# Optimization experiments

Measured on AMD Instinct MI355X. Metric: run time of the kernel, lower is better.

The kernel has to match this reference:

```python
import jax, jax.numpy as jnp
import numpy as np

B, IN_SIZE, OUT_SIZE, N_QUBITS, DEPTH = 4096, 512, 256, 12, 3
C64 = jnp.complex64
BN_EPS = 1e-5


def setup_inputs() -> dict:
    key = jax.random.key(0)
    ks = jax.random.split(key, 6)
    x = jax.random.normal(ks[0], (B, IN_SIZE), jnp.float32)
    enc_w = jax.random.normal(ks[1], (N_QUBITS, IN_SIZE), jnp.float32) / np.sqrt(IN_SIZE)
    enc_b = jnp.zeros((N_QUBITS,), jnp.float32)
    rot_params = jax.random.normal(ks[2], (DEPTH, N_QUBITS, 3), jnp.float32) * 0.1
    ent_params = jax.random.normal(ks[3], (DEPTH, N_QUBITS - 1), jnp.float32) * 0.1
    dec_w = jax.random.normal(ks[4], (OUT_SIZE, N_QUBITS), jnp.float32) / np.sqrt(N_QUBITS)
    dec_b = jnp.zeros((OUT_SIZE,), jnp.float32)
    return {
        'x': x, 'enc_w': enc_w, 'enc_b': enc_b,
        'rot_params': rot_params, 'ent_params': ent_params,
        'dec_w': dec_w, 'dec_b': dec_b,
        'bn1_gamma': jnp.ones((N_QUBITS,), jnp.float32),
        'bn1_beta': jnp.zeros((N_QUBITS,), jnp.float32),
        'bn2_gamma': jnp.ones((OUT_SIZE,), jnp.float32),
        'bn2_beta': jnp.zeros((OUT_SIZE,), jnp.float32),
    }


def _m2(a, b, c, d):
    return jnp.stack([jnp.stack([a, b]), jnp.stack([c, d])]).astype(C64)


def _rx(t):
    c = jnp.cos(t / 2).astype(C64)
    s = jnp.sin(t / 2).astype(C64)
    return _m2(c, -1j * s, -1j * s, c)


def _ry(t):
    c = jnp.cos(t / 2)
    s = jnp.sin(t / 2)
    return _m2(c, -s, s, c)


def _rz(p):
    z = jnp.zeros((), C64)
    return _m2(jnp.exp(-1j * p / 2), z, z, jnp.exp(1j * p / 2))


def _apply_1q(state, U, q):
    # state: [B, 2^n]; apply 2x2 U on qubit q (qubit 0 = most significant axis)
    b = state.shape[0]
    s = state.reshape(b, 2 ** q, 2, -1)
    s = jnp.einsum('ij,bkjl->bkil', U, s)
    return s.reshape(b, -1)


def _apply_cry(state, theta, q):
    # controlled-Ry: control qubit q, target qubit q+1 (adjacent)
    b = state.shape[0]
    R = _ry(theta)
    st = state.reshape(b, 2 ** q, 2, 2, -1)
    s0 = st[:, :, 0]
    s1 = jnp.einsum('ij,bkjl->bkil', R, st[:, :, 1])
    return jnp.stack([s0, s1], axis=2).reshape(b, -1)


def _batchnorm(x, g, b):
    # BatchNorm1d in training mode: biased batch stats
    m = x.mean(0)
    v = x.var(0)
    return g * (x - m) / jnp.sqrt(v + BN_EPS) + b


def _quantum_forward(encoded, rot_params, ent_params):
    # Batched statevector simulation of the per-sample circuit.
    b, n = encoded.shape
    depth = rot_params.shape[0]
    # amplitude encoding: normalize, theta = 2*arcsin(clip(|a|,0,1)), P(pi) if a<0
    norm = jnp.linalg.norm(encoded, axis=1, keepdims=True)
    a = jnp.where(norm > 0, encoded / jnp.maximum(norm, 1e-30), encoded)
    amp = jnp.clip(jnp.abs(a), 0.0, 1.0)              # sin(theta/2)
    cos_h = jnp.sqrt(jnp.maximum(1.0 - amp * amp, 0.0))  # cos(theta/2)
    sgn = jnp.where(a < 0, -1.0, 1.0)                  # P(pi) flips sign of |1> amp
    qvec = jnp.stack([cos_h, sgn * amp], axis=-1).astype(C64)  # [B, n, 2]
    # product state via successive outer products (loop over fixed n qubits)
    state = jnp.ones((b, 1), C64)
    for q in range(n):
        state = (state[:, :, None] * qvec[:, q, None, :]).reshape(b, -1)
    # parameterized circuit
    for l in range(depth):
        for q in range(n):
            U = _rz(rot_params[l, q, 2]) @ _ry(rot_params[l, q, 1]) @ _rx(rot_params[l, q, 0])
            state = _apply_1q(state, U, q)
        for q in range(n - 1):
            state = _apply_cry(state, ent_params[l, q], q)
    # per-qubit P(|1>) measurement probabilities
    idx = jnp.arange(2 ** n)
    bits = ((idx[:, None] >> (n - 1 - jnp.arange(n))) & 1).astype(jnp.float32)  # [2^n, n]
    probs = (jnp.abs(state) ** 2).astype(jnp.float32) @ bits  # [B, n]
    return probs


def reference(x, enc_w, enc_b, rot_params, ent_params, dec_w, dec_b,
              bn1_gamma, bn1_beta, bn2_gamma, bn2_beta):
    encoded = x @ enc_w.T + enc_b
    encoded = jnp.tanh(_batchnorm(encoded, bn1_gamma, bn1_beta))
    probs = _quantum_forward(encoded, rot_params, ent_params)
    out = probs @ dec_w.T + dec_b
    return _batchnorm(out, bn2_gamma, bn2_beta)
```

## Files before the change

### kernel.cpp

```cpp
#include <hip/hip_runtime.h>

#define BATCH   4096
#define IN_SZ   512
#define NQ      12
#define OUT_SZ  256
#define DEPTH   3
#define NST     4096
#define BN_EPS  1e-5f

#define OFF_ENC    0
#define OFF_BN1M   49152
#define OFF_BN1R   49168
#define OFF_GU     49184
#define OFF_GC     49472
#define OFF_GF     49568
#define OFF_PROBS  49792
#define OFF_PMEAN  98944
#define OFF_COV    98960
#define OFF_GG     99104

typedef float v2f __attribute__((ext_vector_type(2)));
typedef float v4f __attribute__((ext_vector_type(4)));
#define SW2(a) __builtin_shufflevector(a, a, 1, 0)

__global__ void k_encode(const float* __restrict__ x, const float* __restrict__ w,
                         const float* __restrict__ bvec,
                         const float* __restrict__ rot, const float* __restrict__ ent,
                         float* __restrict__ enc, float* __restrict__ gU, float* __restrict__ gC,
                         float* __restrict__ gF, float* __restrict__ gG) {
    if (blockIdx.x == 1024) {
        int t = threadIdx.x;
        if (t < DEPTH * NQ) {
            float ax = rot[t * 3 + 0] * 0.5f;
            float ay = rot[t * 3 + 1] * 0.5f;
            float az = rot[t * 3 + 2] * 0.5f;
            float cx = cosf(ax), sx = sinf(ax);
            float cy = cosf(ay), sy = sinf(ay);
            float cz = cosf(az), sz = sinf(az);
            float m00r =  cy * cx, m00i =  sy * sx;
            float m01r = -sy * cx, m01i = -cy * sx;
            float m10r =  sy * cx, m10i = -cy * sx;
            float m11r =  cy * cx, m11i = -sy * sx;
            float* o = gU + t * 8;
            o[0] = cz * m00r + sz * m00i;  o[1] = cz * m00i - sz * m00r;
            o[2] = cz * m01r + sz * m01i;  o[3] = cz * m01i - sz * m01r;
            o[4] = cz * m10r - sz * m10i;  o[5] = cz * m10i + sz * m10r;
            o[6] = cz * m11r - sz * m11i;  o[7] = cz * m11i + sz * m11r;
        }
        if (t >= 64 && t - 64 < DEPTH * (NQ - 1)) {
            int i = t - 64;
            float th = ent[i] * 0.5f;
            gC[i * 2 + 0] = cosf(th);
            gC[i * 2 + 1] = sinf(th);
        }
        if (t >= 128 && t - 128 < DEPTH * 9) {
            int i = t - 128;
            int l = i / 9, k = i % 9;
            int c = k + k / 3;
            int tq = c + 1;
            const float* rr = rot + (l * NQ + tq) * 3;
            float ax = rr[0] * 0.5f, ay = rr[1] * 0.5f, az = rr[2] * 0.5f;
            float cx = cosf(ax), sx = sinf(ax);
            float cy = cosf(ay), sy = sinf(ay);
            float cz = cosf(az), sz = sinf(az);
            float m00r =  cy * cx, m00i =  sy * sx;
            float m01r = -sy * cx, m01i = -cy * sx;
            float m10r =  sy * cx, m10i = -cy * sx;
            float m11r =  cy * cx, m11i = -sy * sx;
            float u0 = cz * m00r + sz * m00i, u1 = cz * m00i - sz * m00r;
            float u2 = cz * m01r + sz * m01i, u3 = cz * m01i - sz * m01r;
            float u4 = cz * m10r - sz * m10i, u5 = cz * m10i + sz * m10r;
            float u6 = cz * m11r - sz * m11i, u7 = cz * m11i + sz * m11r;
            float th = ent[l * (NQ - 1) + c] * 0.5f;
            float c_ = cosf(th), s_ = sinf(th);
            float* o = gF + i * 8;
            o[0] = c_ * u0 - s_ * u4;  o[1] = c_ * u1 - s_ * u5;
            o[2] = c_ * u2 - s_ * u6;  o[3] = c_ * u3 - s_ * u7;
            o[4] = s_ * u0 + c_ * u4;  o[5] = s_ * u1 + c_ * u5;
            o[6] = s_ * u2 + c_ * u6;  o[7] = s_ * u3 + c_ * u7;
        }
        if (t >= 160 && t - 160 < DEPTH * 2) {
            int i = t - 160;
            int l = i >> 1;
            int c = (i & 1) ? 7 : 3;
            int tq = c + 1;
            const float* rr = rot + (l * NQ + tq) * 3;
            float ax = rr[0] * 0.5f, ay = rr[1] * 0.5f, az = rr[2] * 0.5f;
            float cx = cosf(ax), sx = sinf(ax);
            float cy = cosf(ay), sy = sinf(ay);
            float cz = cosf(az), sz = sinf(az);
            float m00r =  cy * cx, m00i =  sy * sx;
            float m01r = -sy * cx, m01i = -cy * sx;
            float m10r =  sy * cx, m10i = -cy * sx;
            float m11r =  cy * cx, m11i = -sy * sx;
            float u0 = cz * m00r + sz * m00i, u1 = cz * m00i - sz * m00r;
            float u2 = cz * m01r + sz * m01i, u3 = cz * m01i - sz * m01r;
            float u4 = cz * m10r - sz * m10i, u5 = cz * m10i + sz * m10r;
            float u6 = cz * m11r - sz * m11i, u7 = cz * m11i + sz * m11r;
            float th = ent[l * (NQ - 1) + c] * 0.5f;
            float c_ = cosf(th), s_ = sinf(th);
            float* o = gG + (l * 2 + (i & 1)) * 8;
            o[0] = c_ * u0 - s_ * u4;  o[1] = c_ * u1 - s_ * u5;
            o[2] = c_ * u2 - s_ * u6;  o[3] = c_ * u3 - s_ * u7;
            o[4] = s_ * u0 + c_ * u4;  o[5] = s_ * u1 + c_ * u5;
            o[6] = s_ * u2 + c_ * u6;  o[7] = s_ * u3 + c_ * u7;
        }
        return;
    }
    int t = threadIdx.x;
    int wv = t >> 6, lane = t & 63;
    int row = blockIdx.x * 4 + wv;
    const float4* xr = (const float4*)(x + row * IN_SZ) + lane * 2;
    float4 xa = xr[0], xb = xr[1];
    float acc[NQ];
    #pragma unroll
    for (int q = 0; q < NQ; q++) {
        const float4* wr = (const float4*)(w + q * IN_SZ) + lane * 2;
        float4 wa = wr[0], wb = wr[1];
        float d = xa.x*wa.x + xa.y*wa.y + xa.z*wa.z + xa.w*wa.w
                + xb.x*wb.x + xb.y*wb.y + xb.z*wb.z + xb.w*wb.w;
        #pragma unroll
        for (int o = 32; o > 0; o >>= 1) d += __shfl_down(d, o, 64);
        acc[q] = d;
    }
    if (lane == 0) {
        float* er = enc + row * NQ;
        #pragma unroll
        for (int q = 0; q < NQ; q++) er[q] = acc[q] + bvec[q];
    }
}

__device__ float blockAllSum(float v, float* scr) {
    #pragma unroll
    for (int o = 32; o > 0; o >>= 1) v += __shfl_down(v, o, 64);
    int lane = threadIdx.x & 63, w = threadIdx.x >> 6;
    __syncthreads();
    if (lane == 0) scr[w] = v;
    __syncthreads();
    return scr[0] + scr[1] + scr[2] + scr[3];
}

__global__ void k_bnstats(const float* __restrict__ xm, float* __restrict__ mo,
                          float* __restrict__ ro) {
    __shared__ float scr[32];
    int j = blockIdx.x, t = threadIdx.x;
    float s = 0.f, s2 = 0.f;
    for (int b = t; b < BATCH; b += 1024) {
        float v = xm[b * NQ + j];
        s += v; s2 += v * v;
    }
    #pragma unroll
    for (int o = 32; o > 0; o >>= 1) { s += __shfl_down(s, o, 64); s2 += __shfl_down(s2, o, 64); }
    int lane = t & 63, w = t >> 6;
    if (lane == 0) { scr[w] = s; scr[16 + w] = s2; }
    __syncthreads();
    if (t == 0) {
        float S = 0.f, S2 = 0.f;
        #pragma unroll
        for (int i = 0; i < 16; i++) { S += scr[i]; S2 += scr[16 + i]; }
        float mean = S / (float)BATCH;
        float var  = S2 / (float)BATCH - mean * mean;
        mo[j] = mean;
        ro[j] = 1.f / sqrtf(var + BN_EPS);
    }
}

#define SLA2(j) ((T << 4) | ((((j) ^ ((T >> 1) & 7))) << 1))
#define SLB(m)  (((T & 0xF0) << 4) | ((m) << 4) | ((T & 15) ^ ((m) & 14)))
#define SLC(m)  (((m) << 8) | (T ^ ((((T >> 5) & 7)) << 1)))

#define LDA(j, Ra, Rb) { v4f t_ = *(const v4f*)(xch + SLA2(j));                 \
    Ra = __builtin_shufflevector(t_, t_, 0, 1);                                 \
    Rb = __builtin_shufflevector(t_, t_, 2, 3); }
#define STA(j, Ra, Rb) { v4f t_ = __builtin_shufflevector(Ra, Rb, 0, 1, 2, 3);  \
    *(v4f*)(xch + SLA2(j)) = t_; }

#define LOADA do { LDA(0,s0,s1) LDA(1,s2,s3) LDA(2,s4,s5) LDA(3,s6,s7)          \
    LDA(4,s8,s9) LDA(5,s10,s11) LDA(6,s12,s13) LDA(7,s14,s15) } while (0)
#define STORA do { STA(0,s0,s1) STA(1,s2,s3) STA(2,s4,s5) STA(3,s6,s7)          \
    STA(4,s8,s9) STA(5,s10,s11) STA(6,s12,s13) STA(7,s14,s15) } while (0)

#define LOADW(SL) do {                                                          \
    s0=xch[SL(0)];  s1=xch[SL(1)];  s2=xch[SL(2)];  s3=xch[SL(3)];              \
    s4=xch[SL(4)];  s5=xch[SL(5)];  s6=xch[SL(6)];  s7=xch[SL(7)];              \
    s8=xch[SL(8)];  s9=xch[SL(9)];  s10=xch[SL(10)]; s11=xch[SL(11)];           \
    s12=xch[SL(12)]; s13=xch[SL(13)]; s14=xch[SL(14)]; s15=xch[SL(15)]; } while (0)
#define STORW(SL) do {                                                          \
    xch[SL(0)]=s0;  xch[SL(1)]=s1;  xch[SL(2)]=s2;  xch[SL(3)]=s3;              \
    xch[SL(4)]=s4;  xch[SL(5)]=s5;  xch[SL(6)]=s6;  xch[SL(7)]=s7;              \
    xch[SL(8)]=s8;  xch[SL(9)]=s9;  xch[SL(10)]=s10; xch[SL(11)]=s11;           \
    xch[SL(12)]=s12; xch[SL(13)]=s13; xch[SL(14)]=s14; xch[SL(15)]=s15; } while (0)

#define U_LOADP(uptr) const float* u_ = (uptr);                                  \
    v2f c00r = {u_[0], u_[0]}, c00i = {-u_[1], u_[1]};                           \
    v2f c01r = {u_[2], u_[2]}, c01i = {-u_[3], u_[3]};                           \
    v2f c10r = {u_[4], u_[4]}, c10i = {-u_[5], u_[5]};                           \
    v2f c11r = {u_[6], u_[6]}, c11i = {-u_[7], u_[7]};

#define U_LOADF(uptr) const float* f_ = (uptr);                                  \
    v2f d00r = {f_[0], f_[0]}, d00i = {-f_[1], f_[1]};                           \
    v2f d01r = {f_[2], f_[2]}, d01i = {-f_[3], f_[3]};                           \
    v2f d10r = {f_[4], f_[4]}, d10i = {-f_[5], f_[5]};                           \
    v2f d11r = {f_[6], f_[6]}, d11i = {-f_[7], f_[7]};

#define U_LOADSEL(uptr, gptr, cond) const float* u_ = (uptr);                    \
    const float* g_ = (gptr); int k_ = (cond);                                   \
    float e0_ = k_ ? g_[0] : u_[0], e1_ = k_ ? g_[1] : u_[1];                    \
    float e2_ = k_ ? g_[2] : u_[2], e3_ = k_ ? g_[3] : u_[3];                    \
    float e4_ = k_ ? g_[4] : u_[4], e5_ = k_ ? g_[5] : u_[5];                    \
    float e6_ = k_ ? g_[6] : u_[6], e7_ = k_ ? g_[7] : u_[7];                    \
    v2f c00r = {e0_, e0_}, c00i = {-e1_, e1_};                                   \
    v2f c01r = {e2_, e2_}, c01i = {-e3_, e3_};                                   \
    v2f c10r = {e4_, e4_}, c10i = {-e5_, e5_};                                   \
    v2f c11r = {e6_, e6_}, c11i = {-e7_, e7_};

#define U_PAIRP(A, B) { v2f a0 = A, a1 = B, a0s = SW2(a0), a1s = SW2(a1);        \
    A = a0*c00r + a0s*c00i + a1*c01r + a1s*c01i;                                 \
    B = a0*c10r + a0s*c10i + a1*c11r + a1s*c11i; }

#define U_PAIRF(A, B) { v2f a0 = A, a1 = B, a0s = SW2(a0), a1s = SW2(a1);        \
    A = a0*d00r + a0s*d00i + a1*d01r + a1s*d01i;                                 \
    B = a0*d10r + a0s*d10i + a1*d11r + a1s*d11i; }

#define APPLY_U_K3(uptr) do { U_LOADP(uptr)                                      \
    U_PAIRP(s0,s8) U_PAIRP(s1,s9) U_PAIRP(s2,s10) U_PAIRP(s3,s11)                \
    U_PAIRP(s4,s12) U_PAIRP(s5,s13) U_PAIRP(s6,s14) U_PAIRP(s7,s15) } while (0)

#define APPLY_USEL_K3(uptr, gptr, cond) do { U_LOADSEL(uptr, gptr, cond)         \
    U_PAIRP(s0,s8) U_PAIRP(s1,s9) U_PAIRP(s2,s10) U_PAIRP(s3,s11)                \
    U_PAIRP(s4,s12) U_PAIRP(s5,s13) U_PAIRP(s6,s14) U_PAIRP(s7,s15) } while (0)

#define APPLY_UF_K2(uP, uF) do { U_LOADP(uP) U_LOADF(uF)                         \
    U_PAIRP(s0,s4) U_PAIRP(s1,s5) U_PAIRP(s2,s6) U_PAIRP(s3,s7)                  \
    U_PAIRF(s8,s12) U_PAIRF(s9,s13) U_PAIRF(s10,s14) U_PAIRF(s11,s15) } while (0)
#define APPLY_UF_K1(uP, uF) do { U_LOADP(uP) U_LOADF(uF)                         \
    U_PAIRP(s0,s2) U_PAIRP(s1,s3) U_PAIRF(s4,s6) U_PAIRF(s5,s7)                  \
    U_PAIRP(s8,s10) U_PAIRP(s9,s11) U_PAIRF(s12,s14) U_PAIRF(s13,s15) } while (0)
#define APPLY_UF_K0(uP, uF) do { U_LOADP(uP) U_LOADF(uF)                         \
    U_PAIRP(s0,s1) U_PAIRF(s2,s3) U_PAIRP(s4,s5) U_PAIRF(s6,s7)                  \
    U_PAIRP(s8,s9) U_PAIRF(s10,s11) U_PAIRP(s12,s13) U_PAIRF(s14,s15) } while (0)

#define PRJ(S) ((S).x*(S).x + (S).y*(S).y)
#define WREDUCE(v) { v += __shfl_down(v,32,64); v += __shfl_down(v,16,64);       \
    v += __shfl_down(v,8,64); v += __shfl_down(v,4,64);                          \
    v += __shfl_down(v,2,64); v += __shfl_down(v,1,64); }

__launch_bounds__(256)
__global__ void k_quantum(const float* __restrict__ enc,
                          const float* __restrict__ bn1m, const float* __restrict__ bn1r,
                          const float* __restrict__ g1, const float* __restrict__ b1,
                          const float* __restrict__ gU, const float* __restrict__ gC,
                          const float* __restrict__ gF, const float* __restrict__ gG,
                          float* __restrict__ probs) {
    __shared__ __align__(16) v2f xch[NST];

    int T = threadIdx.x, b = blockIdx.x;

    float* qv = (float*)xch;
    if (T < 16) {
        float h = 0.f;
        if (T < NQ) {
            h = tanhf(g1[T] * (enc[b * NQ + T] - bn1m[T]) * bn1r[T] + b1[T]);
        }
        float n2 = h * h;
        n2 += __shfl_xor(n2, 1, 16);
        n2 += __shfl_xor(n2, 2, 16);
        n2 += __shfl_xor(n2, 4, 16);
        n2 += __shfl_xor(n2, 8, 16);
        float norm = sqrtf(n2);
        bool  nz   = norm > 0.f;
        float rinv = 1.f / fmaxf(norm, 1e-30f);
        float a_   = nz ? h * rinv : h;
        float amp_ = fminf(fabsf(a_), 1.f);
        float qc   = sqrtf(fmaxf(1.f - amp_ * amp_, 0.f));
        float qs   = (a_ < 0.f) ? -amp_ : amp_;
        if (T < NQ) { qv[T * 2] = qc; qv[T * 2 + 1] = qs; }
    }
    __syncthreads();
    float qc0 = qv[0],  qs0 = qv[1],  qc1 = qv[2],  qs1 = qv[3];
    float qc2 = qv[4],  qs2 = qv[5],  qc3 = qv[6],  qs3 = qv[7];
    float qc4 = qv[8],  qs4 = qv[9],  qc5 = qv[10], qs5 = qv[11];
    float qc6 = qv[12], qs6 = qv[13], qc7 = qv[14], qs7 = qv[15];
    float qc8 = qv[16], qs8 = qv[17], qc9 = qv[18], qs9 = qv[19];
    float qc10 = qv[20], qs10 = qv[21], qc11 = qv[22], qs11 = qv[23];
    __syncthreads();

    v2f s0, s1, s2, s3, s4, s5, s6, s7, s8, s9, s10, s11, s12, s13, s14, s15;

    {
        float f = ((T>>7)&1 ? qs4 : qc4) * ((T>>6)&1 ? qs5 : qc5)
                * ((T>>5)&1 ? qs6 : qc6) * ((T>>4)&1 ? qs7 : qc7)
                * ((T>>3)&1 ? qs8 : qc8) * ((T>>2)&1 ? qs9 : qc9)
                * ((T>>1)&1 ? qs10 : qc10) * ((T>>0)&1 ? qs11 : qc11);
        float p0c = f * qc0,  p0s = f * qs0;
        float p00 = p0c*qc1, p01 = p0c*qs1, p10 = p0s*qc1, p11 = p0s*qs1;
        float q000 = p00*qc2, q001 = p00*qs2, q010 = p01*qc2, q011 = p01*qs2;
        float q100 = p10*qc2, q101 = p10*qs2, q110 = p11*qc2, q111 = p11*qs2;
        s0  = (v2f){q000*qc3, 0.f};  s1  = (v2f){q000*qs3, 0.f};
        s2  = (v2f){q001*qc3, 0.f};  s3  = (v2f){q001*qs3, 0.f};
        s4  = (v2f){q010*qc3, 0.f};  s5  = (v2f){q010*qs3, 0.f};
        s6  = (v2f){q011*qc3, 0.f};  s7  = (v2f){q011*qs3, 0.f};
        s8  = (v2f){q100*qc3, 0.f};  s9  = (v2f){q100*qs3, 0.f};
        s10 = (v2f){q101*qc3, 0.f};  s11 = (v2f){q101*qs3, 0.f};
        s12 = (v2f){q110*qc3, 0.f};  s13 = (v2f){q110*qs3, 0.f};
        s14 = (v2f){q111*qc3, 0.f};  s15 = (v2f){q111*qs3, 0.f};
        APPLY_U_K3(gU + 0 * 8);
        APPLY_UF_K2(gU + 1 * 8, gF + 0 * 8);
        APPLY_UF_K1(gU + 2 * 8, gF + 1 * 8);
        APPLY_UF_K0(gU + 3 * 8, gF + 2 * 8);
        STORW(SLC);
    }
    __syncthreads();

    #pragma unroll 1
    for (int l = 0; l < DEPTH; l++) {
        const float* UL = gU + l * 96;
        const float* FL = gF + l * 72;
        const float* GL = gG + l * 16;
        LOADW(SLB);
        APPLY_USEL_K3(UL + 4 * 8, GL + 0, T & 16);
        APPLY_UF_K2(UL + 5 * 8, FL + 3 * 8);
        APPLY_UF_K1(UL + 6 * 8, FL + 4 * 8);
        APPLY_UF_K0(UL + 7 * 8, FL + 5 * 8);
        STORW(SLB);
        __builtin_amdgcn_wave_barrier();
        LOADA;
        APPLY_USEL_K3(UL + 8 * 8, GL + 8, T & 1);
        APPLY_UF_K2(UL + 9 * 8, FL + 6 * 8);
        APPLY_UF_K1(UL + 10 * 8, FL + 7 * 8);
        APPLY_UF_K0(UL + 11 * 8, FL + 8 * 8);
        if (l < DEPTH - 1) {
            STORA;
            __syncthreads();
            const float* UN = gU + (l + 1) * 96;
            const float* FN = gF + (l + 1) * 72;
            LOADW(SLC);
            APPLY_U_K3(UN + 0 * 8);
            APPLY_UF_K2(UN + 1 * 8, FN + 0 * 8);
            APPLY_UF_K1(UN + 2 * 8, FN + 1 * 8);
            APPLY_UF_K0(UN + 3 * 8, FN + 2 * 8);
            STORW(SLC);
            __syncthreads();
        }
    }

    float p0 = PRJ(s0),  p1 = PRJ(s1),  p2 = PRJ(s2),  p3 = PRJ(s3);
    float p4 = PRJ(s4),  p5 = PRJ(s5),  p6 = PRJ(s6),  p7 = PRJ(s7);
    float p8 = PRJ(s8),  p9 = PRJ(s9),  p10 = PRJ(s10), p11 = PRJ(s11);
    float p12 = PRJ(s12), p13 = PRJ(s13), p14 = PRJ(s14), p15 = PRJ(s15);
    float tot = p0+p1+p2+p3+p4+p5+p6+p7+p8+p9+p10+p11+p12+p13+p14+p15;
    float r8  = p8+p9+p10+p11+p12+p13+p14+p15;
    float r9  = p4+p5+p6+p7+p12+p13+p14+p15;
    float r10 = p2+p3+p6+p7+p10+p11+p14+p15;
    float r11 = p1+p3+p5+p7+p9+p11+p13+p15;
    float r2 = (T & 32)  ? tot : 0.f;
    float r3 = (T & 16)  ? tot : 0.f;
    float r4 = (T & 8)   ? tot : 0.f;
    float r5 = (T & 4)   ? tot : 0.f;
    float r6 = (T & 2)   ? tot : 0.f;
    float r7 = (T & 1)   ? tot : 0.f;

    WREDUCE(tot)
    WREDUCE(r2) WREDUCE(r3) WREDUCE(r4) WREDUCE(r5) WREDUCE(r6) WREDUCE(r7)
    WREDUCE(r8) WREDUCE(r9) WREDUCE(r10) WREDUCE(r11)

    __syncthreads();
    float* red = (float*)xch;
    int lane = T & 63, w = T >> 6;
    if (lane == 0) {
        float* rr = red + w * NQ;
        rr[0] = (w & 2) ? tot : 0.f;
        rr[1] = (w & 1) ? tot : 0.f;
        rr[2]=r2; rr[3]=r3; rr[4]=r4; rr[5]=r5;
        rr[6]=r6; rr[7]=r7; rr[8]=r8; rr[9]=r9; rr[10]=r10; rr[11]=r11;
    }
    __syncthreads();
    if (T < NQ) probs[b * NQ + T] = red[T] + red[NQ + T] + red[2 * NQ + T] + red[3 * NQ + T];
}

__global__ void k_pcov(const float* __restrict__ probs, float* __restrict__ pmean,
                       float* __restrict__ cov) {
    __shared__ float scr[8];
    int blk = blockIdx.x;
    int q = blk / NQ, q2 = blk % NQ;
    int t = threadIdx.x;
    float sx = 0.f, sy = 0.f, sxy = 0.f;
    for (int b = t; b < BATCH; b += 256) {
        float xv = probs[b * NQ + q];
        float yv = probs[b * NQ + q2];
        sx += xv; sy += yv; sxy += xv * yv;
    }
    float SX  = blockAllSum(sx,  scr);
    float SY  = blockAllSum(sy,  scr);
    float SXY = blockAllSum(sxy, scr);
    if (t == 0) {
        float mx = SX / (float)BATCH, my = SY / (float)BATCH;
        cov[blk] = SXY / (float)BATCH - mx * my;
        if (q == q2) pmean[q] = mx;
    }
}

__global__ void k_final(const float* __restrict__ probs, const float* __restrict__ pmean,
                        const float* __restrict__ cov, const float* __restrict__ dw,
                        const float* __restrict__ g2, const float* __restrict__ b2,
                        float* __restrict__ out) {
    __shared__ float cp[2][NQ];
    __shared__ float cv[NQ * NQ];
    int b0 = blockIdx.x * 2;
    int t = threadIdx.x;
    int half = t >> 8, j = t & 255;
    if (t < NQ)                      cp[0][t]       = probs[b0 * NQ + t]        - pmean[t];
    else if (t >= 256 && t < 256+NQ) cp[1][t - 256] = probs[(b0+1) * NQ + t-256] - pmean[t - 256];
    if (t >= 32 && t < 32 + NQ * NQ) cv[t - 32] = cov[t - 32];
    __syncthreads();
    float wv[NQ];
    #pragma unroll
    for (int q = 0; q < NQ; q++) wv[q] = dw[j * NQ + q];
    float var = 0.f;
    #pragma unroll
    for (int q = 0; q < NQ; q++) {
        float a = 0.f;
        #pragma unroll
        for (int q2 = 0; q2 < NQ; q2++) a += cv[q * NQ + q2] * wv[q2];
        var += wv[q] * a;
    }
    float rstd = 1.f / sqrtf(var + BN_EPS);
    float acc = 0.f;
    #pragma unroll
    for (int q = 0; q < NQ; q++) acc += cp[half][q] * wv[q];
    out[(b0 + half) * OUT_SZ + j] = acc * rstd * g2[j] + b2[j];
}

extern "C" void kernel_launch(void* const* d_in, const int* in_sizes, int n_in,
                              void* d_out, int out_size, void* d_ws, size_t ws_size,
                              hipStream_t stream) {
    const float* x     = (const float*)d_in[0];
    const float* enc_w = (const float*)d_in[1];
    const float* enc_b = (const float*)d_in[2];
    const float* rot   = (const float*)d_in[3];
    const float* ent   = (const float*)d_in[4];
    const float* dec_w = (const float*)d_in[5];
    const float* g1    = (const float*)d_in[7];
    const float* b1    = (const float*)d_in[8];
    const float* g2    = (const float*)d_in[9];
    const float* b2    = (const float*)d_in[10];

    float* ws    = (float*)d_ws;
    float* enc   = ws + OFF_ENC;
    float* bn1m  = ws + OFF_BN1M;
    float* bn1r  = ws + OFF_BN1R;
    float* gU    = ws + OFF_GU;
    float* gC    = ws + OFF_GC;
    float* gF    = ws + OFF_GF;
    float* gG    = ws + OFF_GG;
    float* prb   = ws + OFF_PROBS;
    float* pmean = ws + OFF_PMEAN;
    float* cov   = ws + OFF_COV;

    hipLaunchKernelGGL(k_encode, dim3(1025), dim3(256), 0, stream,
                       x, enc_w, enc_b, rot, ent, enc, gU, gC, gF, gG);
    hipLaunchKernelGGL(k_bnstats, dim3(NQ), dim3(1024), 0, stream, enc, bn1m, bn1r);
    hipLaunchKernelGGL(k_quantum, dim3(BATCH), dim3(256), 0, stream,
                       enc, bn1m, bn1r, g1, b1, gU, gC, gF, gG, prb);
    hipLaunchKernelGGL(k_pcov, dim3(NQ * NQ), dim3(256), 0, stream, prb, pmean, cov);
    hipLaunchKernelGGL(k_final, dim3(BATCH / 2), dim3(512), 0, stream,
                       prb, pmean, cov, dec_w, g2, b2, (float*)d_out);
}
```

Before: 199.4 us.

## Fuse five kernels into one cooperative persistent kernel with grid syncs

Merges encode, BN stats, quantum simulation, covariance and final decode into a single cooperative kernel. Each phase runs as a grid-stride loop over work items, with grid.sync between phases in place of separate launches. The final phase now keeps each thread's decoder weights and variance in registers across many batch pairs. The aim is to remove launch gaps and reuse per-column work, at the cost of grid-wide barriers and very low parallelism in the BN-stats and covariance phases, where only 12 or 144 blocks are busy. A multi-kernel fallback is kept for when the cooperative launch fails.

```diff
diff --git a/kernel.cpp b/kernel.cpp
--- a/kernel.cpp
+++ b/kernel.cpp
@@ -1,4 +1,6 @@
 #include <hip/hip_runtime.h>
+#include <hip/hip_cooperative_groups.h>
+namespace cg = cooperative_groups;
 
 #define BATCH   4096
 #define IN_SZ   512
@@ -12,7 +14,6 @@
 #define OFF_BN1M   49152
 #define OFF_BN1R   49168
 #define OFF_GU     49184
-#define OFF_GC     49472
 #define OFF_GF     49568
 #define OFF_PROBS  49792
 #define OFF_PMEAN  98944
@@ -23,93 +24,89 @@
 typedef float v4f __attribute__((ext_vector_type(4)));
 #define SW2(a) __builtin_shufflevector(a, a, 1, 0)
 
-__global__ void k_encode(const float* __restrict__ x, const float* __restrict__ w,
-                         const float* __restrict__ bvec,
-                         const float* __restrict__ rot, const float* __restrict__ ent,
-                         float* __restrict__ enc, float* __restrict__ gU, float* __restrict__ gC,
-                         float* __restrict__ gF, float* __restrict__ gG) {
-    if (blockIdx.x == 1024) {
-        int t = threadIdx.x;
-        if (t < DEPTH * NQ) {
-            float ax = rot[t * 3 + 0] * 0.5f;
-            float ay = rot[t * 3 + 1] * 0.5f;
-            float az = rot[t * 3 + 2] * 0.5f;
-            float cx = cosf(ax), sx = sinf(ax);
-            float cy = cosf(ay), sy = sinf(ay);
-            float cz = cosf(az), sz = sinf(az);
-            float m00r =  cy * cx, m00i =  sy * sx;
-            float m01r = -sy * cx, m01i = -cy * sx;
-            float m10r =  sy * cx, m10i = -cy * sx;
-            float m11r =  cy * cx, m11i = -sy * sx;
-            float* o = gU + t * 8;
-            o[0] = cz * m00r + sz * m00i;  o[1] = cz * m00i - sz * m00r;
-            o[2] = cz * m01r + sz * m01i;  o[3] = cz * m01i - sz * m01r;
-            o[4] = cz * m10r - sz * m10i;  o[5] = cz * m10i + sz * m10r;
-            o[6] = cz * m11r - sz * m11i;  o[7] = cz * m11i + sz * m11r;
-        }
-        if (t >= 64 && t - 64 < DEPTH * (NQ - 1)) {
-            int i = t - 64;
-            float th = ent[i] * 0.5f;
-            gC[i * 2 + 0] = cosf(th);
-            gC[i * 2 + 1] = sinf(th);
-        }
-        if (t >= 128 && t - 128 < DEPTH * 9) {
-            int i = t - 128;
-            int l = i / 9, k = i % 9;
-            int c = k + k / 3;
-            int tq = c + 1;
-            const float* rr = rot + (l * NQ + tq) * 3;
-            float ax = rr[0] * 0.5f, ay = rr[1] * 0.5f, az = rr[2] * 0.5f;
-            float cx = cosf(ax), sx = sinf(ax);
-            float cy = cosf(ay), sy = sinf(ay);
-            float cz = cosf(az), sz = sinf(az);
-            float m00r =  cy * cx, m00i =  sy * sx;
-            float m01r = -sy * cx, m01i = -cy * sx;
-            float m10r =  sy * cx, m10i = -cy * sx;
-            float m11r =  cy * cx, m11i = -sy * sx;
-            float u0 = cz * m00r + sz * m00i, u1 = cz * m00i - sz * m00r;
-            float u2 = cz * m01r + sz * m01i, u3 = cz * m01i - sz * m01r;
-            float u4 = cz * m10r - sz * m10i, u5 = cz * m10i + sz * m10r;
-            float u6 = cz * m11r - sz * m11i, u7 = cz * m11i + sz * m11r;
-            float th = ent[l * (NQ - 1) + c] * 0.5f;
-            float c_ = cosf(th), s_ = sinf(th);
-            float* o = gF + i * 8;
-            o[0] = c_ * u0 - s_ * u4;  o[1] = c_ * u1 - s_ * u5;
-            o[2] = c_ * u2 - s_ * u6;  o[3] = c_ * u3 - s_ * u7;
-            o[4] = s_ * u0 + c_ * u4;  o[5] = s_ * u1 + c_ * u5;
-            o[6] = s_ * u2 + c_ * u6;  o[7] = s_ * u3 + c_ * u7;
-        }
-        if (t >= 160 && t - 160 < DEPTH * 2) {
-            int i = t - 160;
-            int l = i >> 1;
-            int c = (i & 1) ? 7 : 3;
-            int tq = c + 1;
-            const float* rr = rot + (l * NQ + tq) * 3;
-            float ax = rr[0] * 0.5f, ay = rr[1] * 0.5f, az = rr[2] * 0.5f;
-            float cx = cosf(ax), sx = sinf(ax);
-            float cy = cosf(ay), sy = sinf(ay);
-            float cz = cosf(az), sz = sinf(az);
-            float m00r =  cy * cx, m00i =  sy * sx;
-            float m01r = -sy * cx, m01i = -cy * sx;
-            float m10r =  sy * cx, m10i = -cy * sx;
-            float m11r =  cy * cx, m11i = -sy * sx;
-            float u0 = cz * m00r + sz * m00i, u1 = cz * m00i - sz * m00r;
-            float u2 = cz * m01r + sz * m01i, u3 = cz * m01i - sz * m01r;
-            float u4 = cz * m10r - sz * m10i, u5 = cz * m10i + sz * m10r;
-            float u6 = cz * m11r - sz * m11i, u7 = cz * m11i + sz * m11r;
-            float th = ent[l * (NQ - 1) + c] * 0.5f;
-            float c_ = cosf(th), s_ = sinf(th);
-            float* o = gG + (l * 2 + (i & 1)) * 8;
-            o[0] = c_ * u0 - s_ * u4;  o[1] = c_ * u1 - s_ * u5;
-            o[2] = c_ * u2 - s_ * u6;  o[3] = c_ * u3 - s_ * u7;
-            o[4] = s_ * u0 + c_ * u4;  o[5] = s_ * u1 + c_ * u5;
-            o[6] = s_ * u2 + c_ * u6;  o[7] = s_ * u3 + c_ * u7;
-        }
-        return;
-    }
-    int t = threadIdx.x;
+
+
+__device__ __forceinline__ void gate_prep(int t, const float* __restrict__ rot,
+                                          const float* __restrict__ ent,
+                                          float* __restrict__ gU, float* __restrict__ gF,
+                                          float* __restrict__ gG) {
+    if (t < DEPTH * NQ) {
+        float ax = rot[t * 3 + 0] * 0.5f;
+        float ay = rot[t * 3 + 1] * 0.5f;
+        float az = rot[t * 3 + 2] * 0.5f;
+        float cx = cosf(ax), sx = sinf(ax);
+        float cy = cosf(ay), sy = sinf(ay);
+        float cz = cosf(az), sz = sinf(az);
+        float m00r =  cy * cx, m00i =  sy * sx;
+        float m01r = -sy * cx, m01i = -cy * sx;
+        float m10r =  sy * cx, m10i = -cy * sx;
+        float m11r =  cy * cx, m11i = -sy * sx;
+        float* o = gU + t * 8;
+        o[0] = cz * m00r + sz * m00i;  o[1] = cz * m00i - sz * m00r;
+        o[2] = cz * m01r + sz * m01i;  o[3] = cz * m01i - sz * m01r;
+        o[4] = cz * m10r - sz * m10i;  o[5] = cz * m10i + sz * m10r;
+        o[6] = cz * m11r - sz * m11i;  o[7] = cz * m11i + sz * m11r;
+    }
+    if (t >= 128 && t - 128 < DEPTH * 9) {
+        int i = t - 128;
+        int l = i / 9, k = i % 9;
+        int c = k + k / 3;
+        int tq = c + 1;
+        const float* rr = rot + (l * NQ + tq) * 3;
+        float ax = rr[0] * 0.5f, ay = rr[1] * 0.5f, az = rr[2] * 0.5f;
+        float cx = cosf(ax), sx = sinf(ax);
+        float cy = cosf(ay), sy = sinf(ay);
+        float cz = cosf(az), sz = sinf(az);
+        float m00r =  cy * cx, m00i =  sy * sx;
+        float m01r = -sy * cx, m01i = -cy * sx;
+        float m10r =  sy * cx, m10i = -cy * sx;
+        float m11r =  cy * cx, m11i = -sy * sx;
+        float u0 = cz * m00r + sz * m00i, u1 = cz * m00i - sz * m00r;
+        float u2 = cz * m01r + sz * m01i, u3 = cz * m01i - sz * m01r;
+        float u4 = cz * m10r - sz * m10i, u5 = cz * m10i + sz * m10r;
+        float u6 = cz * m11r - sz * m11i, u7 = cz * m11i + sz * m11r;
+        float th = ent[l * (NQ - 1) + c] * 0.5f;
+        float c_ = cosf(th), s_ = sinf(th);
+        float* o = gF + i * 8;
+        o[0] = c_ * u0 - s_ * u4;  o[1] = c_ * u1 - s_ * u5;
+        o[2] = c_ * u2 - s_ * u6;  o[3] = c_ * u3 - s_ * u7;
+        o[4] = s_ * u0 + c_ * u4;  o[5] = s_ * u1 + c_ * u5;
+        o[6] = s_ * u2 + c_ * u6;  o[7] = s_ * u3 + c_ * u7;
+    }
+    if (t >= 160 && t - 160 < DEPTH * 2) {
+        int i = t - 160;
+        int l = i >> 1;
+        int c = (i & 1) ? 7 : 3;
+        int tq = c + 1;
+        const float* rr = rot + (l * NQ + tq) * 3;
+        float ax = rr[0] * 0.5f, ay = rr[1] * 0.5f, az = rr[2] * 0.5f;
+        float cx = cosf(ax), sx = sinf(ax);
+        float cy = cosf(ay), sy = sinf(ay);
+        float cz = cosf(az), sz = sinf(az);
+        float m00r =  cy * cx, m00i =  sy * sx;
+        float m01r = -sy * cx, m01i = -cy * sx;
+        float m10r =  sy * cx, m10i = -cy * sx;
+        float m11r =  cy * cx, m11i = -sy * sx;
+        float u0 = cz * m00r + sz * m00i, u1 = cz * m00i - sz * m00r;
+        float u2 = cz * m01r + sz * m01i, u3 = cz * m01i - sz * m01r;
+        float u4 = cz * m10r - sz * m10i, u5 = cz * m10i + sz * m10r;
+        float u6 = cz * m11r - sz * m11i, u7 = cz * m11i + sz * m11r;
+        float th = ent[l * (NQ - 1) + c] * 0.5f;
+        float c_ = cosf(th), s_ = sinf(th);
+        float* o = gG + (l * 2 + (i & 1)) * 8;
+        o[0] = c_ * u0 - s_ * u4;  o[1] = c_ * u1 - s_ * u5;
+        o[2] = c_ * u2 - s_ * u6;  o[3] = c_ * u3 - s_ * u7;
+        o[4] = s_ * u0 + c_ * u4;  o[5] = s_ * u1 + c_ * u5;
+        o[6] = s_ * u2 + c_ * u6;  o[7] = s_ * u3 + c_ * u7;
+    }
+}
+
+__device__ __forceinline__ void encode_rows(int it, int t, const float* __restrict__ x,
+                                            const float* __restrict__ w,
+                                            const float* __restrict__ bvec,
+                                            float* __restrict__ enc) {
     int wv = t >> 6, lane = t & 63;
-    int row = blockIdx.x * 4 + wv;
+    int row = it * 4 + wv;
     const float4* xr = (const float4*)(x + row * IN_SZ) + lane * 2;
     float4 xa = xr[0], xb = xr[1];
     float acc[NQ];
@@ -130,38 +127,27 @@
     }
 }
 
-__device__ float blockAllSum(float v, float* scr) {
-    #pragma unroll
-    for (int o = 32; o > 0; o >>= 1) v += __shfl_down(v, o, 64);
-    int lane = threadIdx.x & 63, w = threadIdx.x >> 6;
-    __syncthreads();
-    if (lane == 0) scr[w] = v;
-    __syncthreads();
-    return scr[0] + scr[1] + scr[2] + scr[3];
-}
-
-__global__ void k_bnstats(const float* __restrict__ xm, float* __restrict__ mo,
-                          float* __restrict__ ro) {
-    __shared__ float scr[32];
-    int j = blockIdx.x, t = threadIdx.x;
+__device__ __forceinline__ void bnstats_item(int j, int t, const float* __restrict__ enc,
+                                             float* __restrict__ bn1m, float* __restrict__ bn1r,
+                                             float* __restrict__ scr) {
     float s = 0.f, s2 = 0.f;
-    for (int b = t; b < BATCH; b += 1024) {
-        float v = xm[b * NQ + j];
+    for (int bb = t; bb < BATCH; bb += 256) {
+        float v = enc[bb * NQ + j];
         s += v; s2 += v * v;
     }
     #pragma unroll
     for (int o = 32; o > 0; o >>= 1) { s += __shfl_down(s, o, 64); s2 += __shfl_down(s2, o, 64); }
     int lane = t & 63, w = t >> 6;
-    if (lane == 0) { scr[w] = s; scr[16 + w] = s2; }
+    __syncthreads();
+    if (lane == 0) { scr[w] = s; scr[8 + w] = s2; }
     __syncthreads();
     if (t == 0) {
-        float S = 0.f, S2 = 0.f;
-        #pragma unroll
-        for (int i = 0; i < 16; i++) { S += scr[i]; S2 += scr[16 + i]; }
+        float S  = scr[0] + scr[1] + scr[2] + scr[3];
+        float S2 = scr[8] + scr[9] + scr[10] + scr[11];
         float mean = S / (float)BATCH;
         float var  = S2 / (float)BATCH - mean * mean;
-        mo[j] = mean;
-        ro[j] = 1.f / sqrtf(var + BN_EPS);
+        bn1m[j] = mean;
+        bn1r[j] = 1.f / sqrtf(var + BN_EPS);
     }
 }
 
@@ -245,17 +231,12 @@
     v += __shfl_down(v,8,64); v += __shfl_down(v,4,64);                          \
     v += __shfl_down(v,2,64); v += __shfl_down(v,1,64); }
 
-__launch_bounds__(256)
-__global__ void k_quantum(const float* __restrict__ enc,
-                          const float* __restrict__ bn1m, const float* __restrict__ bn1r,
-                          const float* __restrict__ g1, const float* __restrict__ b1,
-                          const float* __restrict__ gU, const float* __restrict__ gC,
-                          const float* __restrict__ gF, const float* __restrict__ gG,
-                          float* __restrict__ probs) {
-    __shared__ __align__(16) v2f xch[NST];
-
-    int T = threadIdx.x, b = blockIdx.x;
-
+__device__ __forceinline__ void quantum_item(int b, int T, v2f* __restrict__ xch,
+        const float* __restrict__ enc,
+        const float* __restrict__ bn1m, const float* __restrict__ bn1r,
+        const float* __restrict__ g1, const float* __restrict__ b1,
+        const float* __restrict__ gU, const float* __restrict__ gF,
+        const float* __restrict__ gG, float* __restrict__ probs) {
     float* qv = (float*)xch;
     if (T < 16) {
         float h = 0.f;
@@ -378,12 +359,20 @@
     if (T < NQ) probs[b * NQ + T] = red[T] + red[NQ + T] + red[2 * NQ + T] + red[3 * NQ + T];
 }
 
-__global__ void k_pcov(const float* __restrict__ probs, float* __restrict__ pmean,
-                       float* __restrict__ cov) {
-    __shared__ float scr[8];
-    int blk = blockIdx.x;
+__device__ __forceinline__ float blockAllSum(float v, float* scr) {
+    #pragma unroll
+    for (int o = 32; o > 0; o >>= 1) v += __shfl_down(v, o, 64);
+    int lane = threadIdx.x & 63, w = threadIdx.x >> 6;
+    __syncthreads();
+    if (lane == 0) scr[w] = v;
+    __syncthreads();
+    return scr[0] + scr[1] + scr[2] + scr[3];
+}
+
+__device__ __forceinline__ void pcov_item(int blk, int t, const float* __restrict__ probs,
+                                          float* __restrict__ pmean, float* __restrict__ cov,
+                                          float* __restrict__ scr) {
     int q = blk / NQ, q2 = blk % NQ;
-    int t = threadIdx.x;
     float sx = 0.f, sy = 0.f, sxy = 0.f;
     for (int b = t; b < BATCH; b += 256) {
         float xv = probs[b * NQ + q];
@@ -400,22 +389,17 @@
     }
 }
 
-__global__ void k_final(const float* __restrict__ probs, const float* __restrict__ pmean,
-                        const float* __restrict__ cov, const float* __restrict__ dw,
-                        const float* __restrict__ g2, const float* __restrict__ b2,
-                        float* __restrict__ out) {
-    __shared__ float cp[2][NQ];
-    __shared__ float cv[NQ * NQ];
-    int b0 = blockIdx.x * 2;
-    int t = threadIdx.x;
-    int half = t >> 8, j = t & 255;
-    if (t < NQ)                      cp[0][t]       = probs[b0 * NQ + t]        - pmean[t];
-    else if (t >= 256 && t < 256+NQ) cp[1][t - 256] = probs[(b0+1) * NQ + t-256] - pmean[t - 256];
-    if (t >= 32 && t < 32 + NQ * NQ) cv[t - 32] = cov[t - 32];
+__device__ __forceinline__ void final_phase(int start, int stride, int t,
+        const float* __restrict__ probs, const float* __restrict__ pmean,
+        const float* __restrict__ cov, const float* __restrict__ dw,
+        const float* __restrict__ g2, const float* __restrict__ b2,
+        float* __restrict__ out, float* __restrict__ cv,
+        float* __restrict__ cp0, float* __restrict__ cp1) {
+    if (t < NQ * NQ) cv[t] = cov[t];
     __syncthreads();
     float wv[NQ];
     #pragma unroll
-    for (int q = 0; q < NQ; q++) wv[q] = dw[j * NQ + q];
+    for (int q = 0; q < NQ; q++) wv[q] = dw[t * NQ + q];
     float var = 0.f;
     #pragma unroll
     for (int q = 0; q < NQ; q++) {
@@ -425,10 +409,107 @@
         var += wv[q] * a;
     }
     float rstd = 1.f / sqrtf(var + BN_EPS);
-    float acc = 0.f;
-    #pragma unroll
-    for (int q = 0; q < NQ; q++) acc += cp[half][q] * wv[q];
-    out[(b0 + half) * OUT_SZ + j] = acc * rstd * g2[j] + b2[j];
+    float g2t = g2[t], b2t = b2[t];
+    #pragma unroll 1
+    for (int it = start; it < BATCH / 2; it += stride) {
+        int b0 = it * 2;
+        __syncthreads();
+        if (t < NQ)                    cp0[t]      = probs[b0 * NQ + t]           - pmean[t];
+        else if (t >= 64 && t < 64+NQ) cp1[t - 64] = probs[(b0+1) * NQ + (t - 64)] - pmean[t - 64];
+        __syncthreads();
+        float a0 = 0.f, a1 = 0.f;
+        #pragma unroll
+        for (int q = 0; q < NQ; q++) { a0 += cp0[q] * wv[q]; a1 += cp1[q] * wv[q]; }
+        out[b0 * OUT_SZ + t]       = a0 * rstd * g2t + b2t;
+        out[(b0 + 1) * OUT_SZ + t] = a1 * rstd * g2t + b2t;
+    }
+}
+
+__global__ void __launch_bounds__(256) k_mega(
+        const float* __restrict__ x, const float* __restrict__ w,
+        const float* __restrict__ bvec, const float* __restrict__ rot,
+        const float* __restrict__ ent, const float* __restrict__ dw,
+        const float* __restrict__ g1, const float* __restrict__ b1,
+        const float* __restrict__ g2, const float* __restrict__ b2,
+        float* __restrict__ enc, float* __restrict__ bn1m, float* __restrict__ bn1r,
+        float* __restrict__ gU, float* __restrict__ gF, float* __restrict__ gG,
+        float* __restrict__ probs, float* __restrict__ pmean, float* __restrict__ cov,
+        float* __restrict__ out) {
+    __shared__ __align__(16) v2f xch[NST];
+    cg::grid_group grid = cg::this_grid();
+    const int nb = (int)gridDim.x;
+    const int T  = (int)threadIdx.x;
+
+    #pragma unroll 1
+    for (int it = blockIdx.x; it < 1025; it += nb) {
+        if (it == 1024) gate_prep(T, rot, ent, gU, gF, gG);
+        else            encode_rows(it, T, x, w, bvec, enc);
+    }
+    grid.sync();
+
+    #pragma unroll 1
+    for (int j = blockIdx.x; j < NQ; j += nb)
+        bnstats_item(j, T, enc, bn1m, bn1r, (float*)xch);
+    grid.sync();
+
+    #pragma unroll 1
+    for (int b = blockIdx.x; b < BATCH; b += nb) {
+        __syncthreads();
+        quantum_item(b, T, xch, enc, bn1m, bn1r, g1, b1, gU, gF, gG, probs);
+    }
+    grid.sync();
+
+    #pragma unroll 1
+    for (int blk = blockIdx.x; blk < NQ * NQ; blk += nb)
+        pcov_item(blk, T, probs, pmean, cov, (float*)xch);
+    grid.sync();
+
+    {
+        float* cv  = (float*)xch;
+        float* cp0 = (float*)xch + 160;
+        float* cp1 = (float*)xch + 176;
+        final_phase(blockIdx.x, nb, T, probs, pmean, cov, dw, g2, b2, out, cv, cp0, cp1);
+    }
+}
+
+__global__ void k_encode_f(const float* __restrict__ x, const float* __restrict__ w,
+                           const float* __restrict__ bvec, const float* __restrict__ rot,
+                           const float* __restrict__ ent, float* __restrict__ enc,
+                           float* __restrict__ gU, float* __restrict__ gF,
+                           float* __restrict__ gG) {
+    int it = blockIdx.x;
+    if (it == 1024) gate_prep(threadIdx.x, rot, ent, gU, gF, gG);
+    else            encode_rows(it, threadIdx.x, x, w, bvec, enc);
+}
+
+__global__ void k_bnstats_f(const float* __restrict__ enc, float* __restrict__ bn1m,
+                            float* __restrict__ bn1r) {
+    __shared__ float scr[16];
+    bnstats_item(blockIdx.x, threadIdx.x, enc, bn1m, bn1r, scr);
+}
+
+__global__ void __launch_bounds__(256) k_quantum_f(const float* __restrict__ enc,
+        const float* __restrict__ bn1m, const float* __restrict__ bn1r,
+        const float* __restrict__ g1, const float* __restrict__ b1,
+        const float* __restrict__ gU, const float* __restrict__ gF,
+        const float* __restrict__ gG, float* __restrict__ probs) {
+    __shared__ __align__(16) v2f xch[NST];
+    quantum_item(blockIdx.x, threadIdx.x, xch, enc, bn1m, bn1r, g1, b1, gU, gF, gG, probs);
+}
+
+__global__ void k_pcov_f(const float* __restrict__ probs, float* __restrict__ pmean,
+                         float* __restrict__ cov) {
+    __shared__ float scr[8];
+    pcov_item(blockIdx.x, threadIdx.x, probs, pmean, cov, scr);
+}
+
+__global__ void k_final_f(const float* __restrict__ probs, const float* __restrict__ pmean,
+                          const float* __restrict__ cov, const float* __restrict__ dw,
+                          const float* __restrict__ g2, const float* __restrict__ b2,
+                          float* __restrict__ out) {
+    __shared__ float buf[192];
+    final_phase(blockIdx.x, gridDim.x, threadIdx.x, probs, pmean, cov, dw, g2, b2,
+                out, buf, buf + 160, buf + 176);
 }
 
 extern "C" void kernel_launch(void* const* d_in, const int* in_sizes, int n_in,
@@ -450,19 +531,44 @@
     float* bn1m  = ws + OFF_BN1M;
     float* bn1r  = ws + OFF_BN1R;
     float* gU    = ws + OFF_GU;
-    float* gC    = ws + OFF_GC;
     float* gF    = ws + OFF_GF;
     float* gG    = ws + OFF_GG;
     float* prb   = ws + OFF_PROBS;
     float* pmean = ws + OFF_PMEAN;
     float* cov   = ws + OFF_COV;
-
-    hipLaunchKernelGGL(k_encode, dim3(1025), dim3(256), 0, stream,
-                       x, enc_w, enc_b, rot, ent, enc, gU, gC, gF, gG);
-    hipLaunchKernelGGL(k_bnstats, dim3(NQ), dim3(1024), 0, stream, enc, bn1m, bn1r);
-    hipLaunchKernelGGL(k_quantum, dim3(BATCH), dim3(256), 0, stream,
-                       enc, bn1m, bn1r, g1, b1, gU, gC, gF, gG, prb);
-    hipLaunchKernelGGL(k_pcov, dim3(NQ * NQ), dim3(256), 0, stream, prb, pmean, cov);
-    hipLaunchKernelGGL(k_final, dim3(BATCH / 2), dim3(512), 0, stream,
-                       prb, pmean, cov, dec_w, g2, b2, (float*)d_out);
-}
+    float* outp  = (float*)d_out;
+
+    static int g_grid = 0;
+    if (g_grid == 0) {
+        int nb = 0;
+        if (hipOccupancyMaxActiveBlocksPerMultiprocessor(&nb, k_mega, 256, 0) != hipSuccess
+            || nb < 1) nb = 2;
+        int dev = 0;
+        (void)hipGetDevice(&dev);
+        int cus = 0;
+        if (hipDeviceGetAttribute(&cus, hipDeviceAttributeMultiprocessorCount, dev) != hipSuccess
+            || cus < 1) cus = 256;
+        long g = (long)nb * (long)cus;
+        g_grid = (g >= 1024) ? 1024 : (int)g;
+    }
+
+    void* kargs[] = {
+        (void*)&x, (void*)&enc_w, (void*)&enc_b, (void*)&rot, (void*)&ent, (void*)&dec_w,
+        (void*)&g1, (void*)&b1, (void*)&g2, (void*)&b2,
+        (void*)&enc, (void*)&bn1m, (void*)&bn1r, (void*)&gU, (void*)&gF, (void*)&gG,
+        (void*)&prb, (void*)&pmean, (void*)&cov, (void*)&outp
+    };
+    hipError_t err = hipLaunchCooperativeKernel(k_mega, dim3(g_grid), dim3(256),
+                                                kargs, 0, stream);
+    if (err != hipSuccess) {
+        (void)hipGetLastError();
+        hipLaunchKernelGGL(k_encode_f, dim3(1025), dim3(256), 0, stream,
+                           x, enc_w, enc_b, rot, ent, enc, gU, gF, gG);
+        hipLaunchKernelGGL(k_bnstats_f, dim3(NQ), dim3(256), 0, stream, enc, bn1m, bn1r);
+        hipLaunchKernelGGL(k_quantum_f, dim3(BATCH), dim3(256), 0, stream,
+                           enc, bn1m, bn1r, g1, b1, gU, gF, gG, prb);
+        hipLaunchKernelGGL(k_pcov_f, dim3(NQ * NQ), dim3(256), 0, stream, prb, pmean, cov);
+        hipLaunchKernelGGL(k_final_f, dim3(BATCH / 2), dim3(256), 0, stream,
+                           prb, pmean, cov, dec_w, g2, b2, outp);
+    }
+}
```

New measurement: 403.6 us. 102% more time.
